# Kernel optimization log

Hardware: AMD Instinct MI355X
Metric: run time of the kernel (lower is better)

The kernel has to match this reference:

```python
import jax, jax.numpy as jnp
import numpy as np

B, C, D_IN, T = 8, 4, 256, 1024
D_MODEL = 256


def setup_inputs() -> dict:
    key = jax.random.key(0)
    k_x, k_m, k_wq, k_bq, k_wo, k_bo = jax.random.split(key, 6)
    x = jax.random.normal(k_x, (B, C, D_IN, T), dtype=jnp.float32)
    mask = jax.random.randint(k_m, (B, C, T, T), 0, 2) == 1  # bool, True = masked
    s_in = 1.0 / np.sqrt(D_IN)
    s_md = 1.0 / np.sqrt(D_MODEL)
    w_qkv = jax.random.uniform(k_wq, (3 * D_MODEL, D_IN), jnp.float32, -s_in, s_in)
    b_qkv = jax.random.uniform(k_bq, (3 * D_MODEL,), jnp.float32, -s_in, s_in)
    w_out = jax.random.uniform(k_wo, (D_MODEL, D_MODEL), jnp.float32, -s_md, s_md)
    b_out = jax.random.uniform(k_bo, (D_MODEL,), jnp.float32, -s_md, s_md)
    return {"x": x, "mask": mask, "w_qkv": w_qkv, "b_qkv": b_qkv,
            "w_out": w_out, "b_out": b_out}


def reference(x, mask, w_qkv, b_qkv, w_out, b_out):
    # x: (B, C, d_in, t) -> (B, C, t, d_in)
    xt = jnp.swapaxes(x, -1, -2)
    qkv = jnp.einsum('bctd,ed->bcte', xt, w_qkv) + b_qkv  # (B,C,t,3*d_model)
    q, k, v = jnp.split(qkv, 3, axis=-1)
    scale = 1.0 / jnp.sqrt(jnp.asarray(q.shape[-1], dtype=q.dtype))
    scores = jnp.einsum('bcqd,bckd->bcqk', q, k) * scale  # (B,C,t,t)
    scores = jnp.where(mask, -jnp.inf, scores)
    attn = jax.nn.softmax(scores, axis=-1)
    out = jnp.einsum('bcqk,bckd->bcqd', attn, v)          # (B,C,t,d_model)
    return jnp.einsum('bcqd,ed->bcqe', out, w_out) + b_out
```

## Files before the change

kernel.cpp:

```cpp
#include <hip/hip_runtime.h>
#include <hip/hip_bf16.h>

#define TT 1024
#define DM 256
#define BCN 32

typedef __attribute__((ext_vector_type(8))) short short8;
typedef __attribute__((ext_vector_type(4))) short short4v;
typedef __attribute__((ext_vector_type(4))) float f32x4;

__device__ __forceinline__ void wg_barrier_lds() {
  asm volatile("s_waitcnt lgkmcnt(0)\n\ts_barrier" ::: "memory");
}

__device__ __forceinline__ short bf16b(float f) {
  __hip_bfloat16 h = __float2bfloat16(f);
  return *(short*)&h;
}

__device__ __forceinline__ void dma16(void* l, const void* g) {
  __builtin_amdgcn_global_load_lds(
      (const __attribute__((address_space(1))) void*)g,
      (__attribute__((address_space(3))) void*)l, 16, 0, 0);
}
__device__ __forceinline__ void dma4(void* l, const void* g) {
  __builtin_amdgcn_global_load_lds(
      (const __attribute__((address_space(1))) void*)g,
      (__attribute__((address_space(3))) void*)l, 4, 0, 0);
}

__global__ __launch_bounds__(256, 2) void qkv_kernel(
    const float* __restrict__ x, const float* __restrict__ w_qkv,
    const float* __restrict__ b_qkv, const int* __restrict__ mask,
    __hip_bfloat16* __restrict__ Qb, __hip_bfloat16* __restrict__ Kb,
    __hip_bfloat16* __restrict__ Vtb, unsigned* __restrict__ mbits)
{
  const int tid = threadIdx.x;

  if (blockIdx.x >= 512) {
    const int g = (blockIdx.x - 512) * 256 + tid;
#pragma unroll
    for (int k = 0; k < 8; ++k) {
      const int word = g + k * 131072;
      const int bc = word >> 15, j = (word >> 10) & 31, q = word & 1023;
      const int4* mp =
          (const int4*)(mask + ((size_t)(bc * 1024 + q) * 1024 + j * 32));
      unsigned w = 0;
#pragma unroll
      for (int i = 0; i < 8; ++i) {
        const int4 v = mp[i];
        w |= ((unsigned)(v.x != 0) << (4 * i)) |
             ((unsigned)(v.y != 0) << (4 * i + 1)) |
             ((unsigned)(v.z != 0) << (4 * i + 2)) |
             ((unsigned)(v.w != 0) << (4 * i + 3));
      }
      mbits[word] = w;
    }
    return;
  }

  const int tt = blockIdx.x & 15, bc = blockIdx.x >> 4;
  const int t0 = tt * 64;

  __shared__ __attribute__((aligned(16))) __hip_bfloat16 Xs[64][264];
  __shared__ __attribute__((aligned(16))) __hip_bfloat16 Ws[64][264];

  const int w = tid >> 6, l = tid & 63, quad = l >> 4, lm = l & 15;
  const float* xbc = x + (size_t)bc * DM * TT;

  {
    const int t4 = (tid & 15) * 4;
    for (int s = 0; s < 4; ++s) {
      const int d4 = (tid >> 4) * 4 + s * 64;
      f32x4 f[4];
#pragma unroll
      for (int r = 0; r < 4; ++r)
        f[r] = *(const f32x4*)(xbc + (size_t)(d4 + r) * TT + t0 + t4);
#pragma unroll
      for (int r = 0; r < 4; ++r) {
        short4v pk;
#pragma unroll
        for (int c = 0; c < 4; ++c) pk[c] = bf16b(f[c][r]);
        *(short4v*)&Xs[t4 + r][d4] = pk;
      }
    }
  }

  const float4* wv4 = (const float4*)w_qkv;

  for (int et = 0; et < 12; ++et) {
    const int e0 = et * 64;
    const bool vmode = (et >= 8);
    wg_barrier_lds();
#pragma unroll
    for (int i = 0; i < 16; ++i) {
      const int idx = tid + i * 256, row = idx >> 6, c4 = idx & 63;
      const float4 f = wv4[(size_t)et * 4096 + idx];
      short4v pk;
      pk[0] = bf16b(f.x); pk[1] = bf16b(f.y);
      pk[2] = bf16b(f.z); pk[3] = bf16b(f.w);
      *(short4v*)&Ws[row][c4 * 4] = pk;
    }
    wg_barrier_lds();

    f32x4 acc[4] = {};
#pragma unroll
    for (int ks = 0; ks < 8; ++ks) {
      const int k = ks * 32 + quad * 8;
      const short8 xa = *(const short8*)&Xs[w * 16 + lm][k];
#pragma unroll
      for (int nt = 0; nt < 4; ++nt) {
        const short8 wb = *(const short8*)&Ws[nt * 16 + lm][k];
        acc[nt] = vmode
            ? __builtin_amdgcn_mfma_f32_16x16x32_bf16(xa, wb, acc[nt], 0, 0, 0)
            : __builtin_amdgcn_mfma_f32_16x16x32_bf16(wb, xa, acc[nt], 0, 0, 0);
      }
    }

    if (et < 4) {
      const int t = t0 + w * 16 + lm;
#pragma unroll
      for (int nt = 0; nt < 4; ++nt) {
        const int ebase = e0 + nt * 16 + quad * 4;
        short4v pk;
#pragma unroll
        for (int r = 0; r < 4; ++r) pk[r] = bf16b(acc[nt][r] + b_qkv[ebase + r]);
        *(short4v*)&Qb[((size_t)bc * TT + t) * DM + ebase] = pk;
      }
    } else if (!vmode) {
      const int t = t0 + w * 16 + lm;
#pragma unroll
      for (int nt = 0; nt < 4; ++nt) {
        const int eg = e0 + nt * 16 + quad * 4;
        const int eK = eg - 256;
        short4v pk;
#pragma unroll
        for (int r = 0; r < 4; ++r) pk[r] = bf16b(acc[nt][r] + b_qkv[eg + r]);
        const int ch = eK >> 3;
        const int off = (((ch ^ (t & 7)) << 3) | (eK & 7));
        *(short4v*)&Kb[((size_t)bc * TT + t) * DM + off] = pk;
      }
    } else {
      const int tb = w * 16 + quad * 4;
      const int kb = tt * 2 + (tb >> 5), tloc = tb & 31;
#pragma unroll
      for (int nt = 0; nt < 4; ++nt) {
        const int e = (e0 - 512) + nt * 16 + lm;
        const float bq = b_qkv[512 + e];
        short4v pk;
#pragma unroll
        for (int r = 0; r < 4; ++r) pk[r] = bf16b(acc[nt][r] + bq);
        *(short4v*)&Vtb[(((size_t)bc * 32 + kb) * 256 + e) * 32 + tloc] = pk;
      }
    }
  }
}

__global__ __launch_bounds__(256, 2) void attn_kernel(
    const __hip_bfloat16* __restrict__ Qb, const __hip_bfloat16* __restrict__ Kb,
    const __hip_bfloat16* __restrict__ Vtb, const unsigned* __restrict__ Mbits,
    __hip_bfloat16* __restrict__ Ob)
{
  const int fid = blockIdx.x;
  const int xcd = fid & 7, slot = fid >> 3;
  const int bc = xcd * 4 + (slot >> 4);
  const int qt = slot & 15;
  const int q0 = qt * 64;

  __shared__ __attribute__((aligned(16))) __hip_bfloat16 Ks[2][32 * 256];
  __shared__ __attribute__((aligned(16))) __hip_bfloat16 Vs[2][256 * 32];
  __shared__ __attribute__((aligned(16))) __hip_bfloat16 Ps[64][40];
  __shared__ unsigned Msb[2][64];

  const int tid = threadIdx.x, w = tid >> 6, l = tid & 63;
  const int quad = l >> 4, lm = l & 15, lm7 = lm & 7;

  const __hip_bfloat16* Qg =
      Qb + ((size_t)bc * TT + q0 + w * 16 + lm) * DM + quad * 8;
  short8 qf[8];
#pragma unroll
  for (int ks = 0; ks < 8; ++ks) qf[ks] = *(const short8*)(Qg + ks * 32);

  const char* KgT = (const char*)(Kb + (size_t)bc * TT * DM);
  const char* VgT = (const char*)(Vtb + (size_t)bc * TT * DM);
  const unsigned* MgT = Mbits + ((size_t)bc * 32) * 1024 + q0;

  short8 ones;
#pragma unroll
  for (int i = 0; i < 8; ++i) ones[i] = (short)0x3F80;

  f32x4 Oa[16] = {};
  f32x4 Ol = {};

  auto issue = [&](int j, int buf) {
    const char* kg = KgT + (size_t)j * 16384 + w * 4096 + l * 16;
    const char* vg = VgT + (size_t)j * 16384 + w * 4096 + l * 16;
    char* kl = (char*)&Ks[buf][0] + w * 4096;
    char* vl = (char*)&Vs[buf][0] + w * 4096;
#pragma unroll
    for (int i = 0; i < 4; ++i) dma16(kl + i * 1024, kg + i * 1024);
#pragma unroll
    for (int i = 0; i < 4; ++i) dma16(vl + i * 1024, vg + i * 1024);
    dma4(&Msb[buf][0], MgT + (size_t)j * 1024 + l);
  };

  auto compute = [&](int buf) {
    const __hip_bfloat16* KT = &Ks[buf][0];
    const __hip_bfloat16* VT = &Vs[buf][0];
    f32x4 Sa0 = {}, Sa1 = {};
#pragma unroll
    for (int ks = 0; ks < 8; ++ks) {
      const int c = ((ks * 4 + quad) ^ lm7) << 3;
      const short8 a0 = *(const short8*)&KT[lm * 256 + c];
      const short8 a1 = *(const short8*)&KT[(lm + 16) * 256 + c];
      Sa0 = __builtin_amdgcn_mfma_f32_16x16x32_bf16(a0, qf[ks], Sa0, 0, 0, 0);
      Sa1 = __builtin_amdgcn_mfma_f32_16x16x32_bf16(a1, qf[ks], Sa1, 0, 0, 0);
    }
    const unsigned mw = Msb[buf][w * 16 + lm];
#pragma unroll
    for (int nt = 0; nt < 2; ++nt) {
      const f32x4 Sa = nt ? Sa1 : Sa0;
      short4v pk;
#pragma unroll
      for (int r = 0; r < 4; ++r) {
        const int jj = nt * 16 + quad * 4 + r;
        const float p = ((mw >> jj) & 1u)
                            ? 0.f
                            : __expf(fmaf(Sa[r], 0.0625f, -8.0f));
        pk[r] = bf16b(p);
      }
      *(short4v*)&Ps[w * 16 + lm][nt * 16 + quad * 4] = pk;
    }
    const short8 pf = *(const short8*)&Ps[w * 16 + lm][quad * 8];
#pragma unroll
    for (int ct = 0; ct < 16; ++ct) {
      const short8 a = *(const short8*)&VT[(ct * 16 + lm) * 32 + quad * 8];
      Oa[ct] = __builtin_amdgcn_mfma_f32_16x16x32_bf16(a, pf, Oa[ct], 0, 0, 0);
    }
    Ol = __builtin_amdgcn_mfma_f32_16x16x32_bf16(ones, pf, Ol, 0, 0, 0);
  };

  issue(0, 0);
  issue(1, 1);
#pragma unroll 1
  for (int j = 0; j < 32; ++j) {
    const int buf = j & 1;
    if (j < 31)
      asm volatile("s_waitcnt vmcnt(9)" ::: "memory");
    else
      asm volatile("s_waitcnt vmcnt(0)" ::: "memory");
    asm volatile("s_barrier" ::: "memory");
    compute(buf);
    wg_barrier_lds();
    if (j < 30) issue(j + 2, buf);
  }

  const float inv = 1.0f / Ol[0];
  __hip_bfloat16* Og = Ob + ((size_t)bc * TT + q0 + w * 16 + lm) * DM;
#pragma unroll
  for (int ct = 0; ct < 16; ++ct) {
    short4v pk;
#pragma unroll
    for (int r = 0; r < 4; ++r) pk[r] = bf16b(Oa[ct][r] * inv);
    *(short4v*)&Og[ct * 16 + quad * 4] = pk;
  }
}

__global__ __launch_bounds__(256, 2) void proj_kernel(
    const __hip_bfloat16* __restrict__ Ob, const float* __restrict__ w_out,
    const float* __restrict__ b_out, float* __restrict__ out)
{
  const int ft = blockIdx.x, tt = blockIdx.y, bc = blockIdx.z;
  const int f0 = ft * 64, t0 = tt * 64;

  __shared__ __attribute__((aligned(16))) __hip_bfloat16 As[64][264];
  __shared__ __attribute__((aligned(16))) __hip_bfloat16 Bs[64][264];

  const int tid = threadIdx.x;
  const uint4* Og4 = (const uint4*)(Ob + ((size_t)bc * TT + t0) * DM);
#pragma unroll
  for (int i = 0; i < 8; ++i) {
    const int chunk = tid + i * 256, row = chunk >> 5, c8 = chunk & 31;
    *(uint4*)&As[row][c8 * 8] = Og4[chunk];
  }
  {
    const float4* wv = (const float4*)(w_out + (size_t)f0 * DM);
#pragma unroll
    for (int i = 0; i < 16; ++i) {
      const int idx = tid + i * 256, row = idx >> 6, c4 = idx & 63;
      const float4 f = wv[idx];
      short4v pk;
      pk[0] = bf16b(f.x); pk[1] = bf16b(f.y);
      pk[2] = bf16b(f.z); pk[3] = bf16b(f.w);
      *(short4v*)&Bs[row][c4 * 4] = pk;
    }
  }
  __syncthreads();

  const int w = tid >> 6, l = tid & 63, quad = l >> 4, lm = l & 15;
  f32x4 acc[4] = {};
#pragma unroll
  for (int ks = 0; ks < 8; ++ks) {
    const int k = ks * 32 + quad * 8;
    const short8 ob = *(const short8*)&As[w * 16 + lm][k];
#pragma unroll
    for (int nt = 0; nt < 4; ++nt) {
      const short8 wa = *(const short8*)&Bs[nt * 16 + lm][k];
      acc[nt] = __builtin_amdgcn_mfma_f32_16x16x32_bf16(wa, ob, acc[nt], 0, 0, 0);
    }
  }
  const int t = t0 + w * 16 + lm;
#pragma unroll
  for (int nt = 0; nt < 4; ++nt) {
    const int fb = f0 + nt * 16 + quad * 4;
    float4 o;
    o.x = acc[nt][0] + b_out[fb + 0];
    o.y = acc[nt][1] + b_out[fb + 1];
    o.z = acc[nt][2] + b_out[fb + 2];
    o.w = acc[nt][3] + b_out[fb + 3];
    *(float4*)&out[((size_t)bc * TT + t) * DM + fb] = o;
  }
}

extern "C" void kernel_launch(void* const* d_in, const int* in_sizes, int n_in,
                              void* d_out, int out_size, void* d_ws, size_t ws_size,
                              hipStream_t stream) {
  const float* x = (const float*)d_in[0];
  const int* mask = (const int*)d_in[1];
  const float* w_qkv = (const float*)d_in[2];
  const float* b_qkv = (const float*)d_in[3];
  const float* w_out = (const float*)d_in[4];
  const float* b_out = (const float*)d_in[5];
  float* out = (float*)d_out;

  const size_t N = (size_t)BCN * TT * DM;
  __hip_bfloat16* Qb  = (__hip_bfloat16*)d_ws;
  __hip_bfloat16* Kb  = Qb + N;
  __hip_bfloat16* Vtb = Kb + N;
  unsigned* Mbits     = (unsigned*)(Vtb + N);

  qkv_kernel<<<dim3(1024), dim3(256), 0, stream>>>(x, w_qkv, b_qkv, mask,
                                                   Qb, Kb, Vtb, Mbits);
  attn_kernel<<<dim3(512), dim3(256), 0, stream>>>(Qb, Kb, Vtb, Mbits, Qb);
  proj_kernel<<<dim3(4, 16, BCN), dim3(256), 0, stream>>>(Qb, w_out, b_out, out);
}
```

Before: 361.7 us.

## Coalesce mask bit-packing with wave ballots and LDS transpose

The mask-packing blocks now read whole mask rows with coalesced int4 loads, prefetching the next row while processing the current one. Bits are gathered with wave ballots into a permuted bit order, staged in LDS (reusing the Xs buffer), then written out transposed. The attention kernel's bit extraction is changed to match the new bit permutation. This targets the strided, uncoalesced reads of the roughly 128 MB int mask in the old packing loop, which likely dominate runtime. The cost is a different block-to-work mapping and a bit layout that both kernels must agree on.

```diff
diff --git a/kernel.cpp b/kernel.cpp
--- a/kernel.cpp
+++ b/kernel.cpp
@@ -37,33 +37,57 @@
 {
   const int tid = threadIdx.x;
 
+  __shared__ __attribute__((aligned(16))) __hip_bfloat16 Xs[64][264];
+  __shared__ __attribute__((aligned(16))) __hip_bfloat16 Ws[64][264];
+
   if (blockIdx.x >= 512) {
-    const int g = (blockIdx.x - 512) * 256 + tid;
-#pragma unroll
-    for (int k = 0; k < 8; ++k) {
-      const int word = g + k * 131072;
-      const int bc = word >> 15, j = (word >> 10) & 31, q = word & 1023;
-      const int4* mp =
-          (const int4*)(mask + ((size_t)(bc * 1024 + q) * 1024 + j * 32));
-      unsigned w = 0;
-#pragma unroll
-      for (int i = 0; i < 8; ++i) {
-        const int4 v = mp[i];
-        w |= ((unsigned)(v.x != 0) << (4 * i)) |
-             ((unsigned)(v.y != 0) << (4 * i + 1)) |
-             ((unsigned)(v.z != 0) << (4 * i + 2)) |
-             ((unsigned)(v.w != 0) << (4 * i + 3));
-      }
-      mbits[word] = w;
+    const int m = blockIdx.x - 512;
+    const int bc = m >> 4, q0 = (m & 15) * 64;
+    unsigned (*Wlds)[33] = (unsigned(*)[33]) & Xs[0][0];
+    const int w = tid >> 6, l = tid & 63;
+    const int4* base =
+        (const int4*)(mask + (size_t)(bc * 1024 + q0 + w * 16) * 1024) + l;
+    int4 v[4], n[4];
+#pragma unroll
+    for (int s = 0; s < 4; ++s) v[s] = base[s * 64];
+#pragma unroll 1
+    for (int rr = 0; rr < 16; ++rr) {
+      if (rr < 15) {
+        const int4* nb = base + (rr + 1) * 256;
+#pragma unroll
+        for (int s = 0; s < 4; ++s) n[s] = nb[s * 64];
+      }
+      const int ql = w * 16 + rr;
+#pragma unroll
+      for (int s = 0; s < 4; ++s) {
+        const unsigned long long bx = __ballot(v[s].x != 0);
+        const unsigned long long by = __ballot(v[s].y != 0);
+        const unsigned long long bz = __ballot(v[s].z != 0);
+        const unsigned long long bw = __ballot(v[s].w != 0);
+        if (l < 8) {
+          const unsigned word =
+              (unsigned)((bx >> (8 * l)) & 0xFF) |
+              ((unsigned)((by >> (8 * l)) & 0xFF) << 8) |
+              ((unsigned)((bz >> (8 * l)) & 0xFF) << 16) |
+              ((unsigned)((bw >> (8 * l)) & 0xFF) << 24);
+          Wlds[ql][s * 8 + l] = word;
+        }
+      }
+#pragma unroll
+      for (int s = 0; s < 4; ++s) v[s] = n[s];
+    }
+    __syncthreads();
+    unsigned* mb = mbits + (size_t)bc * 32 * 1024 + q0;
+#pragma unroll
+    for (int i = 0; i < 8; ++i) {
+      const int idx = tid + i * 256, j = idx >> 6, ql = idx & 63;
+      mb[(size_t)j * 1024 + ql] = Wlds[ql][j];
     }
     return;
   }
 
   const int tt = blockIdx.x & 15, bc = blockIdx.x >> 4;
   const int t0 = tt * 64;
-
-  __shared__ __attribute__((aligned(16))) __hip_bfloat16 Xs[64][264];
-  __shared__ __attribute__((aligned(16))) __hip_bfloat16 Ws[64][264];
 
   const int w = tid >> 6, l = tid & 63, quad = l >> 4, lm = l & 15;
   const float* xbc = x + (size_t)bc * DM * TT;
@@ -223,8 +247,7 @@
       short4v pk;
 #pragma unroll
       for (int r = 0; r < 4; ++r) {
-        const int jj = nt * 16 + quad * 4 + r;
-        const float p = ((mw >> jj) & 1u)
+        const float p = ((mw >> (nt * 4 + quad + 8 * r)) & 1u)
                             ? 0.f
                             : __expf(fmaf(Sa[r], 0.0625f, -8.0f));
         pk[r] = bf16b(p);
```

Result: faster. 350.1 us (-3.2%).
